# Optimization experiments

Hardware: AMD Instinct MI355X
Metric: run time of the kernel (lower is better)

The kernel has to match this reference:

```python
import jax, jax.numpy as jnp
import numpy as np

V, E, H = 32000, 512, 1024
B, TS, TP = 32, 50, 32


def build_sparse_u_input(slot_np):
    # faithful jnp version of get_sparse_selective_input (vocab.decode EOS check skipped)
    ts, b = slot_np.shape
    res = jnp.full((ts, b, V + ts), 1e-10, dtype=jnp.float32)
    copy_mask = (slot_np == 2) | (slot_np >= V)
    add_mask = (slot_np != 0) & (~copy_mask)
    ti = jnp.arange(ts)[:, None]
    bi = jnp.arange(b)[None, :]
    res = res.at[ti, bi, slot_np].add(add_mask.astype(jnp.float32))
    res = res.at[ti, bi, V + ti].add((5.0 - 1e-10) * copy_mask.astype(jnp.float32))
    return jnp.transpose(res, (1, 0, 2))  # [B, Ts, V+Ts]


def setup_inputs() -> dict:
    key = jax.random.key(0)
    ks = jax.random.split(key, 20)
    s = lambda d: 1.0 / np.sqrt(d)
    slot_np = jax.random.randint(ks[0], (TS, B), 0, V)
    inp = {
        'slot_enc_out': jax.random.normal(ks[1], (TS, B, H), jnp.float32),
        'personality_enc_out': jax.random.normal(ks[2], (TP, B, H), jnp.float32),
        'last_hidden': jax.random.normal(ks[3], (1, B, H), jnp.float32),
        'm_t_input': jax.random.randint(ks[4], (1, B), 0, V),
        'slot_np': slot_np,
        'sparse_u_input': build_sparse_u_input(slot_np),
        'emb': jax.random.normal(ks[5], (V, E), jnp.float32),
        'W_attn_a': jax.random.normal(ks[6], (H, 2 * H), jnp.float32) * s(2 * H),
        'b_attn_a': jnp.zeros((H,), jnp.float32),
        'v_a': jax.random.normal(ks[7], (H,), jnp.float32) * s(H),
        'W_attn_p': jax.random.normal(ks[8], (H, 2 * H), jnp.float32) * s(2 * H),
        'b_attn_p': jnp.zeros((H,), jnp.float32),
        'v_p': jax.random.normal(ks[9], (H,), jnp.float32) * s(H),
        'W_ih': jax.random.normal(ks[10], (3 * H, E + 2 * H), jnp.float32) * s(E + 2 * H),
        'W_hh': jax.random.normal(ks[11], (3 * H, H), jnp.float32) * s(H),
        'b_ih': jnp.zeros((3 * H,), jnp.float32),
        'b_hh': jnp.zeros((3 * H,), jnp.float32),
        'W_proj': jax.random.normal(ks[12], (V, 3 * H), jnp.float32) * s(3 * H),
        'b_proj': jnp.zeros((V,), jnp.float32),
        'W_c2': jax.random.normal(ks[13], (H, H), jnp.float32) * s(H),
        'b_c2': jnp.zeros((H,), jnp.float32),
    }
    return inp


def _attn(hidden, enc, W, b, v):
    # hidden: [1,B,H], enc: [T,B,H] -> context [B,H]
    enc_b = jnp.swapaxes(enc, 0, 1)                       # [B,T,H]
    Hh = jnp.broadcast_to(hidden[0][:, None, :], enc_b.shape)
    e = jnp.tanh(jnp.concatenate([Hh, enc_b], -1) @ W.T + b)  # [B,T,H]
    a = jax.nn.softmax(jnp.einsum('bth,h->bt', e, v), axis=-1)
    return jnp.einsum('bt,bth->bh', a, enc_b)


def _gru_cell(x, h, W_ih, W_hh, b_ih, b_hh):
    gi = x @ W_ih.T + b_ih
    gh = h @ W_hh.T + b_hh
    ir, iz, inn = jnp.split(gi, 3, axis=-1)
    hr, hz, hn = jnp.split(gh, 3, axis=-1)
    r = jax.nn.sigmoid(ir + hr)
    z = jax.nn.sigmoid(iz + hz)
    n = jnp.tanh(inn + r * hn)
    return (1.0 - z) * n + z * h


def reference(slot_enc_out, personality_enc_out, last_hidden, m_t_input, slot_np,
              sparse_u_input, emb, W_attn_a, b_attn_a, v_a, W_attn_p, b_attn_p, v_p,
              W_ih, W_hh, b_ih, b_hh, W_proj, b_proj, W_c2, b_c2):
    m_embed = emb[m_t_input[0]]                                    # [B,E]
    a_ctx = _attn(last_hidden, slot_enc_out, W_attn_a, b_attn_a, v_a)
    p_ctx = _attn(last_hidden, personality_enc_out, W_attn_p, b_attn_p, v_p)
    gru_in = jnp.concatenate([m_embed, a_ctx, p_ctx], axis=-1)     # [B,E+2H]
    h_new = _gru_cell(gru_in, last_hidden[0], W_ih, W_hh, b_ih, b_hh)  # [B,H]
    gen_score = jnp.concatenate([a_ctx, p_ctx, h_new], -1) @ W_proj.T + b_proj  # [B,V]
    # copy score
    uc = jnp.tanh(jnp.swapaxes(slot_enc_out, 0, 1) @ W_c2.T + b_c2)  # [B,Ts,H]
    u = jnp.einsum('bth,bh->bt', uc, h_new)                          # [B,Ts]
    m = jnp.max(u, axis=1, keepdims=True)
    u = jnp.exp(u - m)
    u = jnp.log(jnp.einsum('bt,btv->bv', u, sparse_u_input)) + m     # [B,V+Ts]
    scores = jax.nn.softmax(jnp.concatenate([gen_score, u], axis=1), axis=1)
    gen, cp = scores[:, :V], scores[:, V:]
    proba = jnp.concatenate([gen + cp[:, :V], cp[:, V:]], axis=1)    # [B,V+Ts]
    return proba, h_new[None], h_new[None]
```

## Files before the change

kernel.cpp:

```cpp
#include <hip/hip_runtime.h>
#include <math.h>

static constexpr int V_   = 32000;
static constexpr int E_   = 512;
static constexpr int H_   = 1024;
static constexpr int B_   = 32;
static constexpr int TS_  = 50;
static constexpr int TP_  = 32;
static constexpr int VTS  = V_ + TS_;
static constexpr int H3   = 3 * H_;
static constexpr int GIN_ = E_ + 2 * H_;
static constexpr int NS   = 8;
static constexpr int SLE  = (VTS + NS - 1) / NS;
static constexpr int GSL  = V_ / NS;

__global__ void zero_gather(float* __restrict__ extra,
                            const float* __restrict__ emb,
                            const int* __restrict__ mt,
                            float* __restrict__ gx)
{
    const int i = blockIdx.x * 256 + threadIdx.x;
    if (i < B_ * VTS) extra[i] = 0.f;
    if (i < B_ * E_) gx[i] = emb[(size_t)mt[i >> 9] * E_ + (i & 511)];
}

__device__ __forceinline__ void m32v2_tile(
    const float* __restrict__ A, int lda,
    const float* __restrict__ W, int ldw, int wko,
    int klen, int n0, float* __restrict__ po, int N)
{
    __shared__ float As[32][36];
    __shared__ float Ws[32][257];

    const int tid  = threadIdx.x;
    const int lane = tid & 63;
    const int wv   = tid >> 6;
    const int wq   = lane & 7;
    const int wg   = lane >> 3;
    const int am   = tid >> 3;
    const int aq   = tid & 7;

    float acc[8][4];
#pragma unroll
    for (int i = 0; i < 8; ++i)
#pragma unroll
        for (int j = 0; j < 4; ++j) acc[i][j] = 0.f;

    for (int kb = 0; kb < klen; kb += 32) {
        const float4 a4 = *reinterpret_cast<const float4*>(A + (size_t)am * lda + kb + 4 * aq);
        float4 w4[8];
#pragma unroll
        for (int i = 0; i < 8; ++i)
            w4[i] = *reinterpret_cast<const float4*>(
                W + (size_t)(n0 + wv * 64 + i * 8 + wg) * ldw + wko + kb + 4 * wq);
        __syncthreads();
        As[4 * aq + 0][am] = a4.x; As[4 * aq + 1][am] = a4.y;
        As[4 * aq + 2][am] = a4.z; As[4 * aq + 3][am] = a4.w;
#pragma unroll
        for (int i = 0; i < 8; ++i) {
            const int col = wv * 64 + i * 8 + wg;
            Ws[4 * wq + 0][col] = w4[i].x; Ws[4 * wq + 1][col] = w4[i].y;
            Ws[4 * wq + 2][col] = w4[i].z; Ws[4 * wq + 3][col] = w4[i].w;
        }
        __syncthreads();
#pragma unroll 8
        for (int k = 0; k < 32; ++k) {
            const float4 a0 = *reinterpret_cast<const float4*>(&As[k][wv * 8]);
            const float4 a1 = *reinterpret_cast<const float4*>(&As[k][wv * 8 + 4]);
            const float av[8] = {a0.x, a0.y, a0.z, a0.w, a1.x, a1.y, a1.z, a1.w};
            const float w0 = Ws[k][lane];
            const float w1 = Ws[k][lane + 64];
            const float w2 = Ws[k][lane + 128];
            const float w3 = Ws[k][lane + 192];
#pragma unroll
            for (int i = 0; i < 8; ++i) {
                acc[i][0] = fmaf(av[i], w0, acc[i][0]);
                acc[i][1] = fmaf(av[i], w1, acc[i][1]);
                acc[i][2] = fmaf(av[i], w2, acc[i][2]);
                acc[i][3] = fmaf(av[i], w3, acc[i][3]);
            }
        }
    }
#pragma unroll
    for (int i = 0; i < 8; ++i) {
        float* op = po + (size_t)(wv * 8 + i) * N + n0;
#pragma unroll
        for (int j = 0; j < 4; ++j)
            op[lane + 64 * j] = acc[i][j];
    }
}

__global__ __launch_bounds__(256)
void gemm_hid(const float* __restrict__ hid,
              const float* __restrict__ Wa, const float* __restrict__ Wp,
              float* __restrict__ parts)
{
    const int z = blockIdx.z, y = blockIdx.y, n0 = blockIdx.x * 256;
    const float* W = z ? Wp : Wa;
    m32v2_tile(hid + y * 256, H_, W, 2 * H_, y * 256, 256, n0,
               parts + (size_t)(z * 4 + y) * B_ * H_, H_);
}

__global__ __launch_bounds__(256)
void gemm_gru(const float* __restrict__ gx, const float* __restrict__ ctxa,
              const float* __restrict__ ctxp, const float* __restrict__ hid,
              const float* __restrict__ W_ih, const float* __restrict__ W_hh,
              float* __restrict__ parts)
{
    const int y = blockIdx.y, n0 = blockIdx.x * 256;
    const float* A; int lda; const float* W; int ldw; int wko; int klo;
    if (y < 2)       { klo = y * 256;        A = gx;   lda = E_; W = W_ih; ldw = GIN_; wko = klo; }
    else if (y < 6)  { klo = (y - 2) * 256;  A = ctxa; lda = H_; W = W_ih; ldw = GIN_; wko = 512 + klo; }
    else if (y < 10) { klo = (y - 6) * 256;  A = ctxp; lda = H_; W = W_ih; ldw = GIN_; wko = 1536 + klo; }
    else             { klo = (y - 10) * 256; A = hid;  lda = H_; W = W_hh; ldw = H_;   wko = klo; }
    m32v2_tile(A + klo, lda, W, ldw, wko, 256, n0,
               parts + (size_t)y * B_ * H3, H3);
}

__global__ void reduce_gru(const float* __restrict__ parts,
                           const float* __restrict__ b_ih, const float* __restrict__ b_hh,
                           const float* __restrict__ hid,
                           float* __restrict__ hnew,
                           float* __restrict__ o2, float* __restrict__ o3)
{
    const int i = blockIdx.x * 256 + threadIdx.x;
    if (i >= B_ * H_) return;
    const int b = i >> 10, j = i & 1023;
    float gi[3], gh[3];
#pragma unroll
    for (int c = 0; c < 3; ++c) {
        float s = b_ih[c * H_ + j];
        for (int y = 0; y < 10; ++y)
            s += parts[((size_t)y * B_ + b) * H3 + c * H_ + j];
        gi[c] = s;
        float t = b_hh[c * H_ + j];
        for (int y = 10; y < 14; ++y)
            t += parts[((size_t)y * B_ + b) * H3 + c * H_ + j];
        gh[c] = t;
    }
    const float r = 1.f / (1.f + expf(-(gi[0] + gh[0])));
    const float z = 1.f / (1.f + expf(-(gi[1] + gh[1])));
    const float n = tanhf(gi[2] + r * gh[2]);
    const float o = (1.f - z) * n + z * hid[i];
    hnew[i] = o; o2[i] = o; o3[i] = o;
}

__global__ __launch_bounds__(256)
void gemm_proj(const float* __restrict__ ctxa, const float* __restrict__ ctxp,
               const float* __restrict__ hnew, const float* __restrict__ W_proj,
               float* __restrict__ parts)
{
    const int y = blockIdx.y, n0 = blockIdx.x * 256;
    const int slice = y >> 1, khalf = y & 1;
    const float* A = (slice == 0) ? ctxa : (slice == 1) ? ctxp : hnew;
    m32v2_tile(A + khalf * 512, H_, W_proj, H3, slice * 1024 + khalf * 512,
               512, n0, parts + (size_t)y * B_ * V_, V_);
}

__global__ __launch_bounds__(256)
void gemm_tall84(const float* __restrict__ slot_enc, const float* __restrict__ pers_enc,
                 const float* __restrict__ W_attn_a, const float* __restrict__ W_attn_p,
                 const float* __restrict__ W_c2,
                 const float* __restrict__ b_attn_a, const float* __restrict__ b_attn_p,
                 const float* __restrict__ b_c2,
                 const float* __restrict__ v_a, const float* __restrict__ v_p,
                 const float* __restrict__ parts,
                 float* __restrict__ SA, float* __restrict__ SP, float* __restrict__ UCt)
{
    __shared__ float As[32][68];
    __shared__ float Ws[32][132];
    const int z = blockIdx.z;
    const float* A; const float* W; float* C; int M, ldw;
    if (z == 0)      { A = slot_enc; W = W_attn_a + H_; C = SA;  M = TS_ * B_; ldw = 2 * H_; }
    else if (z == 1) { A = pers_enc; W = W_attn_p + H_; C = SP;  M = TP_ * B_; ldw = 2 * H_; }
    else             { A = slot_enc; W = W_c2;          C = UCt; M = TS_ * B_; ldw = H_; }
    const int m0 = blockIdx.x * 64;
    if (m0 >= M) return;
    const int n0 = blockIdx.y * 128;
    const int tid = threadIdx.x;
    const int tym = tid >> 5;
    const int txn = tid & 31;
    const int sr = tid & 63, sh = tid >> 6;
    const int wr = tid & 127, wh = tid >> 7;

    float acc[8][4];
#pragma unroll
    for (int i = 0; i < 8; ++i)
#pragma unroll
        for (int j = 0; j < 4; ++j) acc[i][j] = 0.f;

    for (int kb = 0; kb < H_; kb += 32) {
        float4 a4[2], w4[4];
#pragma unroll
        for (int q = 0; q < 2; ++q)
            a4[q] = *reinterpret_cast<const float4*>(A + (size_t)(m0 + sr) * H_ + kb + 8 * sh + 4 * q);
#pragma unroll
        for (int q = 0; q < 4; ++q)
            w4[q] = *reinterpret_cast<const float4*>(W + (size_t)(n0 + wr) * ldw + kb + 16 * wh + 4 * q);
        __syncthreads();
#pragma unroll
        for (int q = 0; q < 2; ++q) {
            As[8 * sh + 4 * q + 0][sr] = a4[q].x; As[8 * sh + 4 * q + 1][sr] = a4[q].y;
            As[8 * sh + 4 * q + 2][sr] = a4[q].z; As[8 * sh + 4 * q + 3][sr] = a4[q].w;
        }
#pragma unroll
        for (int q = 0; q < 4; ++q) {
            Ws[16 * wh + 4 * q + 0][wr] = w4[q].x; Ws[16 * wh + 4 * q + 1][wr] = w4[q].y;
            Ws[16 * wh + 4 * q + 2][wr] = w4[q].z; Ws[16 * wh + 4 * q + 3][wr] = w4[q].w;
        }
        __syncthreads();
#pragma unroll 8
        for (int k = 0; k < 32; ++k) {
            const float4 a0 = *reinterpret_cast<const float4*>(&As[k][8 * tym]);
            const float4 a1 = *reinterpret_cast<const float4*>(&As[k][8 * tym + 4]);
            const float av[8] = {a0.x, a0.y, a0.z, a0.w, a1.x, a1.y, a1.z, a1.w};
            const float w0 = Ws[k][txn];
            const float w1 = Ws[k][txn + 32];
            const float w2 = Ws[k][txn + 64];
            const float w3 = Ws[k][txn + 96];
#pragma unroll
            for (int i = 0; i < 8; ++i) {
                acc[i][0] = fmaf(av[i], w0, acc[i][0]);
                acc[i][1] = fmaf(av[i], w1, acc[i][1]);
                acc[i][2] = fmaf(av[i], w2, acc[i][2]);
                acc[i][3] = fmaf(av[i], w3, acc[i][3]);
            }
        }
    }

    if (z < 2) {
        const float* bvec = z ? b_attn_p : b_attn_a;
        const float* vvec = z ? v_p : v_a;
        const float* pp = parts + (size_t)(z * 4) * B_ * H_;
#pragma unroll
        for (int i = 0; i < 8; ++i) {
            const int row = m0 + 8 * tym + i;
            const int b = row & 31;
#pragma unroll
            for (int j = 0; j < 4; ++j) {
                const int col = n0 + txn + 32 * j;
                float ha = bvec[col];
#pragma unroll
                for (int ss = 0; ss < 4; ++ss)
                    ha += pp[((size_t)ss * B_ + b) * H_ + col];
                C[(size_t)row * H_ + col] = tanhf(acc[i][j] + ha) * vvec[col];
            }
        }
    } else {
#pragma unroll
        for (int i = 0; i < 8; ++i) {
            const int row = m0 + 8 * tym + i;
#pragma unroll
            for (int j = 0; j < 4; ++j) {
                const int col = n0 + txn + 32 * j;
                C[(size_t)row * H_ + col] = tanhf(acc[i][j] + b_c2[col]);
            }
        }
    }
}

__global__ __launch_bounds__(512)
void attn_fused2(const float* __restrict__ SA, const float* __restrict__ SP,
                 const float* __restrict__ slot_enc, const float* __restrict__ pers_enc,
                 float* __restrict__ ctxa, float* __restrict__ ctxp)
{
    const int b = blockIdx.x, z = blockIdx.y;
    const int T = z ? TP_ : TS_;
    const float* S   = z ? SP : SA;
    const float* enc = z ? pers_enc : slot_enc;
    float* ctx       = z ? ctxp : ctxa;

    const int tid  = threadIdx.x;
    const int wave = tid >> 6;
    const int lane = tid & 63;
    __shared__ float sc[64];
    __shared__ float aw[64];

    for (int t = wave; t < T; t += 8) {
        const float* e = S + ((size_t)t * B_ + b) * H_;
        float p = 0.f;
        for (int j = lane; j < H_; j += 64) p += e[j];
#pragma unroll
        for (int off = 32; off > 0; off >>= 1) p += __shfl_down(p, off);
        if (lane == 0) sc[t] = p;
    }
    __syncthreads();
    if (tid < 64) {
        const float x = (tid < T) ? sc[tid] : -3.4e38f;
        float mx = x;
#pragma unroll
        for (int off = 32; off > 0; off >>= 1) mx = fmaxf(mx, __shfl_xor(mx, off));
        const float ex = (tid < T) ? expf(x - mx) : 0.f;
        float sm = ex;
#pragma unroll
        for (int off = 32; off > 0; off >>= 1) sm += __shfl_xor(sm, off);
        aw[tid] = ex / sm;
    }
    __syncthreads();
    for (int k = tid; k < H_; k += 512) {
        float c = 0.f;
        for (int t = 0; t < T; ++t)
            c += aw[t] * enc[((size_t)t * B_ + b) * H_ + k];
        ctx[(size_t)b * H_ + k] = c;
    }
}

__global__ __launch_bounds__(512)
void u_prep_scatter2(const float* __restrict__ UCt, const float* __restrict__ hn,
                     const int* __restrict__ slot_np,
                     float* __restrict__ mS, float* __restrict__ extra)
{
    const int b    = blockIdx.x;
    const int tid  = threadIdx.x;
    const int wave = tid >> 6;
    const int lane = tid & 63;
    __shared__ float su[64];
    __shared__ float eu_s[64];

    const float* h = hn + (size_t)b * H_;
    for (int t = wave; t < TS_; t += 8) {
        const float* r = UCt + ((size_t)t * B_ + b) * H_;
        float p = 0.f;
        for (int j = lane; j < H_; j += 64)
            p += r[j] * h[j];
#pragma unroll
        for (int off = 32; off > 0; off >>= 1) p += __shfl_down(p, off);
        if (lane == 0) su[t] = p;
    }
    __syncthreads();
    if (tid < 64) {
        const float x = (tid < TS_) ? su[tid] : -3.4e38f;
        float mx = x;
#pragma unroll
        for (int off = 32; off > 0; off >>= 1) mx = fmaxf(mx, __shfl_xor(mx, off));
        const float ex = (tid < TS_) ? expf(x - mx) : 0.f;
        float sm = ex;
#pragma unroll
        for (int off = 32; off > 0; off >>= 1) sm += __shfl_xor(sm, off);
        eu_s[tid] = ex;
        if (tid == 0) { mS[b * 2] = mx; mS[b * 2 + 1] = sm; }
    }
    __syncthreads();
    if (tid < TS_) {
        const int sv = slot_np[tid * B_ + b];
        const float e = eu_s[tid];
        const bool copy = (sv == 2) || (sv >= V_);
        const bool add  = (sv != 0) && !copy;
        if (add)  atomicAdd(&extra[(size_t)b * VTS + sv], e);
        if (copy) atomicAdd(&extra[(size_t)b * VTS + V_ + tid], 5.0f * e);
    }
}

__device__ __forceinline__ float blk_reduce(float v, float* red, int tid, bool ismax)
{
    red[tid] = v; __syncthreads();
    for (int s = 128; s > 0; s >>= 1) {
        if (tid < s) red[tid] = ismax ? fmaxf(red[tid], red[tid + s]) : (red[tid] + red[tid + s]);
        __syncthreads();
    }
    const float r = red[0]; __syncthreads();
    return r;
}

__global__ __launch_bounds__(256)
void ph_max2g(const float* __restrict__ parts, const float* __restrict__ b_proj,
              const float* __restrict__ extra,
              float* __restrict__ gen,
              float* __restrict__ pgm, float* __restrict__ pzs,
              float* __restrict__ pem, float* __restrict__ pes)
{
    const int b = blockIdx.x, s = blockIdx.y, tid = threadIdx.x;
    __shared__ float red[256];
    const int g0 = s * GSL;

    float gv[16];
    float gm = -3.4e38f;
#pragma unroll
    for (int u = 0; u < 16; ++u) {
        const int loc = tid + 256 * u;
        float val = -3.4e38f;
        if (loc < GSL) {
            const int idx = g0 + loc;
            float ssum = 0.f;
#pragma unroll
            for (int ss = 0; ss < 6; ++ss)
                ssum += parts[((size_t)ss * B_ + b) * V_ + idx];
            val = ssum + b_proj[idx];
            gen[(size_t)b * V_ + idx] = val;
            gm = fmaxf(gm, val);
        }
        gv[u] = val;
    }
    gm = blk_reduce(gm, red, tid, true);
    float zs = 0.f;
#pragma unroll
    for (int u = 0; u < 16; ++u)
        zs += expf(gv[u] - gm);
    zs = blk_reduce(zs, red, tid, false);

    const float* ex = extra + (size_t)b * VTS;
    const int e0 = s * SLE;
    const int e1 = (e0 + SLE < VTS) ? e0 + SLE : VTS;
    float em = 0.f, es = 0.f;
    for (int i = e0 + tid; i < e1; i += 256) { const float v = ex[i]; em = fmaxf(em, v); es += v; }
    em = blk_reduce(em, red, tid, true);
    es = blk_reduce(es, red, tid, false);
    if (tid == 0) {
        pgm[b * NS + s] = gm; pzs[b * NS + s] = zs;
        pem[b * NS + s] = em; pes[b * NS + s] = es;
    }
}

__global__ __launch_bounds__(256)
void ph_write2(const float* __restrict__ gen, const float* __restrict__ extra,
               const float* __restrict__ pgm, const float* __restrict__ pzs,
               const float* __restrict__ pem, const float* __restrict__ pes,
               const float* __restrict__ mS, float* __restrict__ proba)
{
    const int b = blockIdx.x, s = blockIdx.y, tid = threadIdx.x;
    const float mb   = mS[b * 2];
    const float Sb   = mS[b * 2 + 1];
    const float base = 1e-10f * Sb;

    float gm = -3.4e38f, em = 0.f;
#pragma unroll
    for (int k = 0; k < NS; ++k) {
        gm = fmaxf(gm, pgm[b * NS + k]);
        em = fmaxf(em, pem[b * NS + k]);
    }
    const float M = fmaxf(gm, mb + logf(base + em));
    float s1 = 0.f, s2 = 0.f;
#pragma unroll
    for (int k = 0; k < NS; ++k) {
        s1 += pzs[b * NS + k] * expf(pgm[b * NS + k] - M);
        s2 += pes[b * NS + k];
    }
    const float cs  = expf(mb - M);
    const float inv = 1.f / (s1 + cs * (base * VTS + s2));

    const float* g  = gen + (size_t)b * V_;
    const float* ex = extra + (size_t)b * VTS;
    float* o = proba + (size_t)b * VTS;
    const int e0 = s * SLE;
    const int e1 = (e0 + SLE < VTS) ? e0 + SLE : VTS;
    for (int i = e0 + tid; i < e1; i += 256) {
        const float cp = cs * (base + ex[i]) * inv;
        o[i] = (i < V_) ? (expf(g[i] - M) * inv + cp) : cp;
    }
}

extern "C" void kernel_launch(void* const* d_in, const int* in_sizes, int n_in,
                              void* d_out, int out_size, void* d_ws, size_t ws_size,
                              hipStream_t stream)
{
    const float* slot_enc = (const float*)d_in[0];
    const float* pers_enc = (const float*)d_in[1];
    const float* hid      = (const float*)d_in[2];
    const int*   mt       = (const int*)d_in[3];
    const int*   slot_np  = (const int*)d_in[4];
    const float* emb      = (const float*)d_in[6];
    const float* W_attn_a = (const float*)d_in[7];
    const float* b_attn_a = (const float*)d_in[8];
    const float* v_a      = (const float*)d_in[9];
    const float* W_attn_p = (const float*)d_in[10];
    const float* b_attn_p = (const float*)d_in[11];
    const float* v_p      = (const float*)d_in[12];
    const float* W_ih     = (const float*)d_in[13];
    const float* W_hh     = (const float*)d_in[14];
    const float* b_ih     = (const float*)d_in[15];
    const float* b_hh     = (const float*)d_in[16];
    const float* W_proj   = (const float*)d_in[17];
    const float* b_proj   = (const float*)d_in[18];
    const float* W_c2     = (const float*)d_in[19];
    const float* b_c2     = (const float*)d_in[20];
    float* out = (float*)d_out;

    float* w = (float*)d_ws;
    size_t off = 0;
    auto alloc = [&](size_t n) { float* p = w + off; off += n; return p; };
    float* SA    = alloc((size_t)TS_ * B_ * H_);
    float* SP    = alloc((size_t)TP_ * B_ * H_);
    float* UCt   = alloc((size_t)TS_ * B_ * H_);
    float* ctxa  = alloc((size_t)B_ * H_);
    float* ctxp  = alloc((size_t)B_ * H_);
    float* gx    = alloc((size_t)B_ * E_);
    float* hnew  = alloc((size_t)B_ * H_);
    float* gen   = alloc((size_t)B_ * V_);
    float* mS    = alloc((size_t)2 * B_);
    float* extra = alloc((size_t)B_ * VTS);
    float* pgm   = alloc((size_t)B_ * NS);
    float* pzs   = alloc((size_t)B_ * NS);
    float* pem   = alloc((size_t)B_ * NS);
    float* pes   = alloc((size_t)B_ * NS);
    float* parts = w + off;

    const int o2 = B_ * VTS;
    const int o3 = o2 + B_ * H_;

    zero_gather<<<(B_ * VTS + 255) / 256, 256, 0, stream>>>(extra, emb, mt, gx);

    gemm_hid<<<dim3(4, 4, 2), 256, 0, stream>>>(hid, W_attn_a, W_attn_p, parts);

    gemm_tall84<<<dim3(25, 8, 3), 256, 0, stream>>>(
        slot_enc, pers_enc, W_attn_a, W_attn_p, W_c2,
        b_attn_a, b_attn_p, b_c2, v_a, v_p, parts, SA, SP, UCt);

    attn_fused2<<<dim3(B_, 2), 512, 0, stream>>>(SA, SP, slot_enc, pers_enc, ctxa, ctxp);

    gemm_gru<<<dim3(12, 14), 256, 0, stream>>>(gx, ctxa, ctxp, hid, W_ih, W_hh, parts);
    reduce_gru<<<(B_ * H_ + 255) / 256, 256, 0, stream>>>(parts, b_ih, b_hh, hid, hnew, out + o2, out + o3);

    gemm_proj<<<dim3(125, 6), 256, 0, stream>>>(ctxa, ctxp, hnew, W_proj, parts);

    u_prep_scatter2<<<B_, 512, 0, stream>>>(UCt, hnew, slot_np, mS, extra);

    ph_max2g<<<dim3(B_, NS), 256, 0, stream>>>(parts, b_proj, extra, gen, pgm, pzs, pem, pes);
    ph_write2<<<dim3(B_, NS), 256, 0, stream>>>(gen, extra, pgm, pzs, pem, pes, mS, out);
}
```

Before: 481.8 us.

## Prefetch next K tile into registers and split projection GEMM K four ways

Both shared-memory GEMM tiles now load the next K slice into registers while the current slice is being computed, so global memory latency overlaps the FMA loop. The vocabulary projection GEMM splits K into quarters instead of halves, doubling the grid to 12 partial slices, and the reduction kernel sums 12 partials. This is meant to raise occupancy and bandwidth use on the large W_proj read. In exchange it writes and reads twice as much partial-sum traffic, and the parts buffer must be large enough.

Result: faster. 471.2 us (-2.2%).

```diff
diff --git a/kernel.cpp b/kernel.cpp
--- a/kernel.cpp
+++ b/kernel.cpp
@@ -13,6 +13,7 @@
 static constexpr int NS   = 8;
 static constexpr int SLE  = (VTS + NS - 1) / NS;
 static constexpr int GSL  = V_ / NS;
+static constexpr int PSK  = 12;
 
 __global__ void zero_gather(float* __restrict__ extra,
                             const float* __restrict__ emb,
@@ -46,13 +47,14 @@
 #pragma unroll
         for (int j = 0; j < 4; ++j) acc[i][j] = 0.f;
 
+    float4 a4 = *reinterpret_cast<const float4*>(A + (size_t)am * lda + 4 * aq);
+    float4 w4[8];
+#pragma unroll
+    for (int i = 0; i < 8; ++i)
+        w4[i] = *reinterpret_cast<const float4*>(
+            W + (size_t)(n0 + wv * 64 + i * 8 + wg) * ldw + wko + 4 * wq);
+
     for (int kb = 0; kb < klen; kb += 32) {
-        const float4 a4 = *reinterpret_cast<const float4*>(A + (size_t)am * lda + kb + 4 * aq);
-        float4 w4[8];
-#pragma unroll
-        for (int i = 0; i < 8; ++i)
-            w4[i] = *reinterpret_cast<const float4*>(
-                W + (size_t)(n0 + wv * 64 + i * 8 + wg) * ldw + wko + kb + 4 * wq);
         __syncthreads();
         As[4 * aq + 0][am] = a4.x; As[4 * aq + 1][am] = a4.y;
         As[4 * aq + 2][am] = a4.z; As[4 * aq + 3][am] = a4.w;
@@ -63,6 +65,13 @@
             Ws[4 * wq + 2][col] = w4[i].z; Ws[4 * wq + 3][col] = w4[i].w;
         }
         __syncthreads();
+        if (kb + 32 < klen) {
+            a4 = *reinterpret_cast<const float4*>(A + (size_t)am * lda + kb + 32 + 4 * aq);
+#pragma unroll
+            for (int i = 0; i < 8; ++i)
+                w4[i] = *reinterpret_cast<const float4*>(
+                    W + (size_t)(n0 + wv * 64 + i * 8 + wg) * ldw + wko + kb + 32 + 4 * wq);
+        }
 #pragma unroll 8
         for (int k = 0; k < 32; ++k) {
             const float4 a0 = *reinterpret_cast<const float4*>(&As[k][wv * 8]);
@@ -151,10 +160,10 @@
                float* __restrict__ parts)
 {
     const int y = blockIdx.y, n0 = blockIdx.x * 256;
-    const int slice = y >> 1, khalf = y & 1;
+    const int slice = y >> 2, kq = y & 3;
     const float* A = (slice == 0) ? ctxa : (slice == 1) ? ctxp : hnew;
-    m32v2_tile(A + khalf * 512, H_, W_proj, H3, slice * 1024 + khalf * 512,
-               512, n0, parts + (size_t)y * B_ * V_, V_);
+    m32v2_tile(A + kq * 256, H_, W_proj, H3, slice * 1024 + kq * 256,
+               256, n0, parts + (size_t)y * B_ * V_, V_);
 }
 
 __global__ __launch_bounds__(256)
@@ -189,14 +198,15 @@
 #pragma unroll
         for (int j = 0; j < 4; ++j) acc[i][j] = 0.f;
 
+    float4 a4[2], w4[4];
+#pragma unroll
+    for (int q = 0; q < 2; ++q)
+        a4[q] = *reinterpret_cast<const float4*>(A + (size_t)(m0 + sr) * H_ + 8 * sh + 4 * q);
+#pragma unroll
+    for (int q = 0; q < 4; ++q)
+        w4[q] = *reinterpret_cast<const float4*>(W + (size_t)(n0 + wr) * ldw + 16 * wh + 4 * q);
+
     for (int kb = 0; kb < H_; kb += 32) {
-        float4 a4[2], w4[4];
-#pragma unroll
-        for (int q = 0; q < 2; ++q)
-            a4[q] = *reinterpret_cast<const float4*>(A + (size_t)(m0 + sr) * H_ + kb + 8 * sh + 4 * q);
-#pragma unroll
-        for (int q = 0; q < 4; ++q)
-            w4[q] = *reinterpret_cast<const float4*>(W + (size_t)(n0 + wr) * ldw + kb + 16 * wh + 4 * q);
         __syncthreads();
 #pragma unroll
         for (int q = 0; q < 2; ++q) {
@@ -209,6 +219,14 @@
             Ws[16 * wh + 4 * q + 2][wr] = w4[q].z; Ws[16 * wh + 4 * q + 3][wr] = w4[q].w;
         }
         __syncthreads();
+        if (kb + 32 < H_) {
+#pragma unroll
+            for (int q = 0; q < 2; ++q)
+                a4[q] = *reinterpret_cast<const float4*>(A + (size_t)(m0 + sr) * H_ + kb + 32 + 8 * sh + 4 * q);
+#pragma unroll
+            for (int q = 0; q < 4; ++q)
+                w4[q] = *reinterpret_cast<const float4*>(W + (size_t)(n0 + wr) * ldw + kb + 32 + 16 * wh + 4 * q);
+        }
 #pragma unroll 8
         for (int k = 0; k < 32; ++k) {
             const float4 a0 = *reinterpret_cast<const float4*>(&As[k][8 * tym]);
@@ -383,7 +401,7 @@
             const int idx = g0 + loc;
             float ssum = 0.f;
 #pragma unroll
-            for (int ss = 0; ss < 6; ++ss)
+            for (int ss = 0; ss < PSK; ++ss)
                 ssum += parts[((size_t)ss * B_ + b) * V_ + idx];
             val = ssum + b_proj[idx];
             gen[(size_t)b * V_ + idx] = val;
@@ -510,7 +528,7 @@
     gemm_gru<<<dim3(12, 14), 256, 0, stream>>>(gx, ctxa, ctxp, hid, W_ih, W_hh, parts);
     reduce_gru<<<(B_ * H_ + 255) / 256, 256, 0, stream>>>(parts, b_ih, b_hh, hid, hnew, out + o2, out + o3);
 
-    gemm_proj<<<dim3(125, 6), 256, 0, stream>>>(ctxa, ctxp, hnew, W_proj, parts);
+    gemm_proj<<<dim3(125, PSK), 256, 0, stream>>>(ctxa, ctxp, hnew, W_proj, parts);
 
     u_prep_scatter2<<<B_, 512, 0, stream>>>(UCt, hnew, slot_np, mS, extra);
 
```
